# Performance work log

Hardware: AMD Instinct MI355X
Metric: run time of the kernel (lower is better)

Reference implementation:

```python
import jax, jax.numpy as jnp
import numpy as np

EMBED = 512; HEADS = 16; WIN = 8; SHIFT = 4

def _rel_pos_index(Wh, Ww):
    # WindowMSA.double_step_seq + transpose-sum + flip(1)
    seq1 = np.arange(0, (2 * Ww - 1) * Wh, 2 * Ww - 1)
    seq2 = np.arange(0, Ww)
    coords = (seq1[:, None] + seq2[None, :]).reshape(1, -1)
    idx = coords + coords.T            # (Wh*Ww, Wh*Ww)
    return idx[:, ::-1].copy()

def _attn_mask(H_pad, W_pad, win, shift, nf):
    # static (trace-time) shifted-window mask, values in {0, -100}
    img = np.zeros((H_pad, W_pad))
    cnt = 0
    for h in (slice(0, -win), slice(-win, -shift), slice(-shift, None)):
        for w in (slice(0, -win), slice(-win, -shift), slice(-shift, None)):
            img[h, w] = cnt
            cnt += 1
    mw = img.reshape(H_pad // win, win, W_pad // win, win).transpose(0, 2, 1, 3).reshape(-1, win * win)
    am = mw[:, None, :] - mw[:, :, None]
    am = np.where(am != 0, -100.0, 0.0)
    return np.tile(am, (1, 1, nf))     # (nW, N, nf*N)

def setup_inputs():
    key = jax.random.key(0)
    ks = jax.random.split(key, 8)
    B, H, W, C, nf = 8, 128, 128, EMBED, 2
    s = 0.02
    return {
        'q': jax.random.normal(ks[0], (B, H * W, C), jnp.float32),
        'kv': jax.random.normal(ks[1], (B, nf, H * W, C), jnp.float32),
        'H': H, 'W': W,
        'rpb_table': jax.random.normal(ks[2], ((2 * WIN - 1) ** 2, HEADS), jnp.float32) * s,
        'Wq': jax.random.normal(ks[3], (C, C), jnp.float32) * s,
        'bq': jnp.zeros((C,), jnp.float32),
        'Wkv': jax.random.normal(ks[4], (C, 2 * C), jnp.float32) * s,
        'bkv': jnp.zeros((2 * C,), jnp.float32),
        'Wo': jax.random.normal(ks[5], (C, C), jnp.float32) * s,
        'bo': jnp.zeros((C,), jnp.float32),
    }

def reference(q, kv, H, W, rpb_table, Wq, bq, Wkv, bkv, Wo, bo):
    B, L, C = q.shape
    nf = kv.shape[1]
    win, shift, heads = WIN, SHIFT, HEADS
    hd = C // heads
    scale = hd ** -0.5
    pad_b = (-H) % win
    pad_r = (-W) % win
    x = q.reshape(B, H, W, C)
    kvx = kv.reshape(B * nf, H, W, C)
    x = jnp.pad(x, ((0, 0), (0, pad_b), (0, pad_r), (0, 0)))
    kvx = jnp.pad(kvx, ((0, 0), (0, pad_b), (0, pad_r), (0, 0)))
    Hp, Wp = H + pad_b, W + pad_r
    nh, nw = Hp // win, Wp // win
    if shift > 0:
        x = jnp.roll(x, (-shift, -shift), (1, 2))
        kvx = jnp.roll(kvx, (-shift, -shift), (1, 2))
        mask = jnp.asarray(_attn_mask(Hp, Wp, win, shift, nf), q.dtype)
    else:
        mask = None
    Nq = win * win
    Nk = nf * Nq
    # window partition: (B, Hp, Wp, C) -> (B*nh*nw, Nq, C)
    qw = x.reshape(B, nh, win, nw, win, C).transpose(0, 1, 3, 2, 4, 5).reshape(B * nh * nw, Nq, C)
    # kv: (B*nf, Hp, Wp, C) -> (B*nh*nw, nf*Nq, C)
    kvw = kvx.reshape(B, nf, nh, win, nw, win, C).transpose(0, 2, 4, 1, 3, 5, 6).reshape(B * nh * nw, Nk, C)
    Bw = qw.shape[0]
    qh = (qw @ Wq + bq).reshape(Bw, Nq, heads, hd).transpose(0, 2, 1, 3) * scale
    kvp = (kvw @ Wkv + bkv).reshape(Bw, Nk, 2, heads, hd).transpose(2, 0, 3, 1, 4)
    kh, vh = kvp[0], kvp[1]
    attn = jnp.einsum('bhqd,bhkd->bhqk', qh, kh)
    rpi = jnp.asarray(_rel_pos_index(win, win).reshape(-1))
    rpb = rpb_table[rpi].reshape(Nq, Nq, heads).transpose(2, 0, 1)  # (heads, Nq, Nq)
    attn = attn + jnp.tile(rpb, (1, 1, nf))[None]
    if mask is not None:
        nW = mask.shape[0]
        attn = (attn.reshape(Bw // nW, nW, heads, Nq, Nk) + mask[None, :, None]).reshape(Bw, heads, Nq, Nk)
    attn = jax.nn.softmax(attn, axis=-1)
    ow = jnp.einsum('bhqk,bhkd->bqhd', attn, vh).reshape(Bw, Nq, C)
    ow = ow @ Wo + bo
    # window reverse
    x = ow.reshape(B, nh, nw, win, win, C).transpose(0, 1, 3, 2, 4, 5).reshape(B, Hp, Wp, C)
    if shift > 0:
        x = jnp.roll(x, (shift, shift), (1, 2))
    x = x[:, :H, :W, :].reshape(B, H * W, C)
    return x
```

## Files before the change

kernel.cpp:

```cpp
#include <hip/hip_runtime.h>

typedef unsigned short ushort_t;
typedef short bf16x8 __attribute__((ext_vector_type(8)));
typedef float f32x4 __attribute__((ext_vector_type(4)));

#define MFMA16(a, b, c) __builtin_amdgcn_mfma_f32_16x16x32_bf16(a, b, c, 0, 0, 0)

static __device__ __forceinline__ float bf2f(ushort_t u) {
  union { unsigned int i; float f; } v;
  v.i = ((unsigned int)u) << 16;
  return v.f;
}
static __device__ __forceinline__ ushort_t f2bf(float f) {
  union { float f; unsigned int i; } v;
  v.f = f;
  unsigned int u = v.i;
  u = u + 0x7fffu + ((u >> 16) & 1u);
  return (ushort_t)(u >> 16);
}
static __device__ __forceinline__ unsigned int cvtpk(float lo, float hi) {
  unsigned int r;
  asm("v_cvt_pk_bf16_f32 %0, %1, %2" : "=v"(r) : "v"(lo), "v"(hi));
  return r;
}
static __device__ __forceinline__ void gload16(const void* g, void* l) {
  __builtin_amdgcn_global_load_lds((const __attribute__((address_space(1))) void*)g,
                                   (__attribute__((address_space(3))) void*)l,
                                   16, 0, 0);
}

__global__ void ws_sentinel(float* out, unsigned long long ws) {
  if (blockIdx.x == 0 && threadIdx.x == 0)
    out[0] = 1.0e6f * (1.0f + (float)(ws >> 23));
}

__global__ __launch_bounds__(256) void wtrans3(const float* __restrict__ Wq,
                                               const float* __restrict__ Wkv,
                                               const float* __restrict__ Wo,
                                               ushort_t* __restrict__ WqT,
                                               ushort_t* __restrict__ WkvT,
                                               ushort_t* __restrict__ WoT) {
  int idx = blockIdx.x * 256 + threadIdx.x;
  if (idx < 262144) {
    int r = idx >> 9, c = idx & 511;
    WqT[c * 512 + r] = f2bf(Wq[idx]);
  } else if (idx < 786432) {
    int i = idx - 262144;
    int r = i >> 10, c = i & 1023;
    WkvT[c * 512 + r] = f2bf(Wkv[i]);
  } else if (idx < 1048576) {
    int i = idx - 786432;
    int r = i >> 9, c = i & 511;
    WoT[c * 512 + r] = f2bf(Wo[i]);
  }
}

template <bool AF32, bool CF32>
__global__ __launch_bounds__(256, 2) void gemm_bt(const void* __restrict__ Av,
                                                  const ushort_t* __restrict__ Bt,
                                                  const float* __restrict__ bias,
                                                  void* __restrict__ Cv,
                                                  int N, int Nt, float cscale) {
  constexpr int K = 512;
  constexpr int NT = K / 32;
  __shared__ __align__(16) ushort_t As[2][128 * 32];
  __shared__ __align__(16) ushort_t Bs[2][128 * 32];
  const int t = threadIdx.x;
  const int l = t & 63;
  const int w = t >> 6;
  const int w32 = w * 32;
  const int wr = w >> 1, wc = w & 1;
  const int lrow = l & 15;
  const int g = l >> 4;

  const int bid = blockIdx.x;
  const int xcd = bid & 7;
  const int slot = bid >> 3;
  const int mt = xcd + 8 * (slot / Nt);
  const int nt = slot % Nt;
  const long m0 = (long)mt * 128;
  const int n0 = nt * 128;

  const int srow = l >> 2;
  const int sseg = l & 3;
  const int swz = ((srow & 3) << 3);
  const int bcol = (sseg * 8) ^ swz;
  const int acolw = (sseg * 8) ^ swz;

  auto stageB = [&](int buf, int kk) {
#pragma unroll
    for (int i = 0; i < 2; i++) {
      const ushort_t* gp = Bt + (long)(n0 + w32 + i * 16 + srow) * K + kk + bcol;
      gload16(gp, &Bs[buf][(w32 + i * 16) * 32]);
    }
  };
  auto loadA = [&](int kk, f32x4* xf, bf16x8* xb) {
    if constexpr (AF32) {
#pragma unroll
      for (int i = 0; i < 2; i++) {
        const float* gp = (const float*)Av + (m0 + w32 + i * 16 + srow) * (long)K + kk + sseg * 8;
        xf[2 * i] = *(const f32x4*)gp;
        xf[2 * i + 1] = *(const f32x4*)(gp + 4);
      }
    } else {
#pragma unroll
      for (int i = 0; i < 2; i++) {
        const ushort_t* gp = (const ushort_t*)Av + (m0 + w32 + i * 16 + srow) * (long)K + kk + sseg * 8;
        xb[i] = *(const bf16x8*)gp;
      }
    }
  };
  auto writeA = [&](int buf, const f32x4* xf, const bf16x8* xb) {
    if constexpr (AF32) {
#pragma unroll
      for (int i = 0; i < 2; i++) {
        union { unsigned int u[4]; bf16x8 v; } r;
        r.u[0] = cvtpk(xf[2 * i][0], xf[2 * i][1]);
        r.u[1] = cvtpk(xf[2 * i][2], xf[2 * i][3]);
        r.u[2] = cvtpk(xf[2 * i + 1][0], xf[2 * i + 1][1]);
        r.u[3] = cvtpk(xf[2 * i + 1][2], xf[2 * i + 1][3]);
        *(bf16x8*)&As[buf][(w32 + i * 16 + srow) * 32 + acolw] = r.v;
      }
    } else {
#pragma unroll
      for (int i = 0; i < 2; i++)
        *(bf16x8*)&As[buf][(w32 + i * 16 + srow) * 32 + acolw] = xb[i];
    }
  };

  const f32x4 fz = {0.f, 0.f, 0.f, 0.f};
  f32x4 acc[4][4];
#pragma unroll
  for (int i = 0; i < 4; i++)
#pragma unroll
    for (int j = 0; j < 4; j++) acc[i][j] = fz;

  {
#pragma unroll
    for (int tt = 0; tt < 2; tt++) {
      const int kk = tt * 32;
      if constexpr (AF32) {
        f32x4 xf[4];
        loadA(kk, xf, nullptr);
        writeA(tt, xf, nullptr);
      } else {
        bf16x8 xb[2];
        loadA(kk, nullptr, xb);
        writeA(tt, nullptr, xb);
      }
      stageB(tt, kk);
    }
    __syncthreads();
  }

  f32x4 axf[2][4];
  bf16x8 axb[2][2];
  loadA(2 * 32, axf[0], axb[0]);

#pragma unroll
  for (int ts = 0; ts < NT; ++ts) {
    const int cur = ts & 1;
    const int pw = ts & 1;
    const int pl = (ts + 1) & 1;

    if (ts + 3 < NT) loadA((ts + 3) * 32, axf[pl], axb[pl]);

    bf16x8 af[4], bfr[4];
#pragma unroll
    for (int mi = 0; mi < 4; mi++) {
      const int aR = wr * 64 + mi * 16 + lrow;
      af[mi] = *(const bf16x8*)&As[cur][aR * 32 + ((g * 8) ^ ((aR & 3) << 3))];
    }
#pragma unroll
    for (int ni = 0; ni < 4; ni++) {
      const int bR = wc * 64 + ni * 16 + lrow;
      bfr[ni] = *(const bf16x8*)&Bs[cur][bR * 32 + ((g * 8) ^ ((bR & 3) << 3))];
    }
    __builtin_amdgcn_s_setprio(1);
#pragma unroll
    for (int mi = 0; mi < 4; mi++)
#pragma unroll
      for (int ni = 0; ni < 4; ni++)
        acc[mi][ni] = MFMA16(af[mi], bfr[ni], acc[mi][ni]);
    __builtin_amdgcn_s_setprio(0);

    __builtin_amdgcn_sched_barrier(0);
    __builtin_amdgcn_s_barrier();
    __builtin_amdgcn_sched_barrier(0);

    if (ts + 2 < NT) {
      writeA(cur, axf[pw], axb[pw]);
      stageB(cur, (ts + 2) * 32);
      if (ts + 3 < NT) {
        if constexpr (AF32) asm volatile("s_waitcnt vmcnt(6) lgkmcnt(0)" ::: "memory");
        else                asm volatile("s_waitcnt vmcnt(4) lgkmcnt(0)" ::: "memory");
      } else {
        asm volatile("s_waitcnt vmcnt(2) lgkmcnt(0)" ::: "memory");
      }
    } else {
      asm volatile("s_waitcnt vmcnt(0) lgkmcnt(0)" ::: "memory");
    }
    __builtin_amdgcn_sched_barrier(0);
    __builtin_amdgcn_s_barrier();
    __builtin_amdgcn_sched_barrier(0);
  }

#pragma unroll
  for (int mi = 0; mi < 4; mi++) {
    const long row0 = m0 + wr * 64 + mi * 16 + (l >> 4) * 4;
#pragma unroll
    for (int ni = 0; ni < 4; ni++) {
      const int col = n0 + wc * 64 + ni * 16 + lrow;
      const float bv = bias[col];
      if constexpr (CF32) {
#pragma unroll
        for (int r = 0; r < 4; r++)
          ((float*)Cv)[(row0 + r) * N + col] = (acc[mi][ni][r] + bv) * cscale;
      } else {
#pragma unroll
        for (int r = 0; r < 4; r += 2) {
          const float a0 = (acc[mi][ni][r] + bv) * cscale;
          const float a1 = (acc[mi][ni][r + 1] + bv) * cscale;
          const unsigned int pk = cvtpk(a0, a1);
          ((ushort_t*)Cv)[(row0 + r) * N + col] = (ushort_t)(pk & 0xffffu);
          ((ushort_t*)Cv)[(row0 + r + 1) * N + col] = (ushort_t)(pk >> 16);
        }
      }
    }
  }
}

__global__ __launch_bounds__(256, 1) void attn_k(const ushort_t* __restrict__ Qp,
                                                 const ushort_t* __restrict__ KVp,
                                                 const float* __restrict__ rpbt,
                                                 ushort_t* __restrict__ Ao) {
  __shared__ ushort_t P[64 * 136];
  __shared__ ushort_t Ks[128 * 32];
  __shared__ ushort_t Vt[32 * 136];
  __shared__ float Ltab[225];
  const int t = threadIdx.x;
  const int l = t & 63;
  const int w = t >> 6;
  const int wnd = blockIdx.x;
  const int h = blockIdx.y;
  const int b = wnd >> 8;
  const int wh = (wnd >> 4) & 15;
  const int ww = wnd & 15;

  const int lrow = l & 15;
  const int lq = l >> 4;
  const int lk = lq * 8;

  auto qrow = [&](int q) -> long {
    int i = q >> 3, j = q & 7;
    int ho = (wh * 8 + i + 4) & 127;
    int wo = (ww * 8 + j + 4) & 127;
    return (long)((b << 14) + (ho << 7) + wo);
  };
  auto kvrow = [&](int kp) -> long {
    int f = kp >> 6, m = kp & 63;
    int i = m >> 3, j = m & 7;
    int ho = (wh * 8 + i + 4) & 127;
    int wo = (ww * 8 + j + 4) & 127;
    return (long)(((b * 2 + f) << 14) + (ho << 7) + wo);
  };
  auto cnt_of = [&](int m) -> int {
    int hr = wh * 8 + (m >> 3), wr2 = ww * 8 + (m & 7);
    int rh = hr < 120 ? 0 : (hr < 124 ? 1 : 2);
    int rw = wr2 < 120 ? 0 : (wr2 < 124 ? 1 : 2);
    return rh * 3 + rw;
  };
  auto cvec = [](int m) -> int { return 15 * (m >> 3) + (m & 7); };

#pragma unroll
  for (int i = 0; i < 2; i++) {
    const int row = w * 32 + i * 16 + (l >> 2);
    const ushort_t* gp = KVp + kvrow(row) * 1024 + h * 32 + (l & 3) * 8;
    gload16(gp, Ks + (w * 32 + i * 16) * 32);
  }
  {
    const int vkp = t & 127;
    const int vdh = t >> 7;
    const ushort_t* vsrc = KVp + kvrow(vkp) * 1024 + 512 + h * 32 + vdh * 16;
    bf16x8 v0 = *(const bf16x8*)(vsrc);
    bf16x8 v1 = *(const bf16x8*)(vsrc + 8);
#pragma unroll
    for (int d = 0; d < 8; d++) {
      Vt[(vdh * 16 + d) * 136 + vkp] = (ushort_t)v0[d];
      Vt[(vdh * 16 + 8 + d) * 136 + vkp] = (ushort_t)v1[d];
    }
  }
  for (int i = t; i < 225; i += 256) Ltab[i] = rpbt[i * 16 + h];

  bf16x8 af = *(const bf16x8*)(Qp + qrow(w * 16 + lrow) * 512 + h * 32 + lk);

  int ck[8], lidx[8];
#pragma unroll
  for (int ni = 0; ni < 8; ni++) {
    const int k63 = (ni * 16 + lrow) & 63;
    ck[ni] = cnt_of(k63);
    lidx[ni] = cvec(63 - k63);
  }
  int cq4[4], cqv4[4];
#pragma unroll
  for (int r = 0; r < 4; r++) {
    const int q = w * 16 + lq * 4 + r;
    cq4[r] = cnt_of(q);
    cqv4[r] = cvec(q);
  }

  __syncthreads();

  const f32x4 fz = {0.f, 0.f, 0.f, 0.f};
  f32x4 s[8];
#pragma unroll
  for (int ni = 0; ni < 8; ni++) s[ni] = fz;
#pragma unroll
  for (int ni = 0; ni < 8; ni++) {
    bf16x8 kf = *(const bf16x8*)&Ks[(ni * 16 + lrow) * 32 + lk];
    s[ni] = MFMA16(af, kf, s[ni]);
  }

  float inv4[4];
#pragma unroll
  for (int r = 0; r < 4; r++) {
    float mx = -3.0e38f;
#pragma unroll
    for (int ni = 0; ni < 8; ni++) {
      float v = s[ni][r] + Ltab[cqv4[r] + lidx[ni]];
      if (ck[ni] != cq4[r]) v -= 100.f;
      s[ni][r] = v;
      mx = fmaxf(mx, v);
    }
    mx = fmaxf(mx, __shfl_xor(mx, 1));
    mx = fmaxf(mx, __shfl_xor(mx, 2));
    mx = fmaxf(mx, __shfl_xor(mx, 4));
    mx = fmaxf(mx, __shfl_xor(mx, 8));
    float sum = 0.f;
#pragma unroll
    for (int ni = 0; ni < 8; ni++) {
      float p = __expf(s[ni][r] - mx);
      s[ni][r] = p;
      sum += p;
    }
    sum += __shfl_xor(sum, 1);
    sum += __shfl_xor(sum, 2);
    sum += __shfl_xor(sum, 4);
    sum += __shfl_xor(sum, 8);
    inv4[r] = 1.f / sum;
    const int q = w * 16 + lq * 4 + r;
#pragma unroll
    for (int ni = 0; ni < 8; ni += 2) {
      const unsigned int pk = cvtpk(s[ni][r], s[ni + 1][r]);
      P[q * 136 + ni * 16 + lrow] = (ushort_t)(pk & 0xffffu);
      P[q * 136 + (ni + 1) * 16 + lrow] = (ushort_t)(pk >> 16);
    }
  }


  f32x4 o[2] = {fz, fz};
#pragma unroll
  for (int ks = 0; ks < 4; ks++) {
    bf16x8 pf = *(const bf16x8*)&P[(w * 16 + lrow) * 136 + ks * 32 + lk];
#pragma unroll
    for (int ni = 0; ni < 2; ni++) {
      bf16x8 vf = *(const bf16x8*)&Vt[(ni * 16 + lrow) * 136 + ks * 32 + lk];
      o[ni] = MFMA16(pf, vf, o[ni]);
    }
  }

#pragma unroll
  for (int ni = 0; ni < 2; ni++)
#pragma unroll
    for (int r = 0; r < 4; r += 2) {
      const unsigned int pk = cvtpk(o[ni][r] * inv4[r], o[ni][r + 1] * inv4[r + 1]);
      const int q0 = w * 16 + lq * 4 + r;
      Ao[qrow(q0) * 512 + h * 32 + ni * 16 + lrow] = (ushort_t)(pk & 0xffffu);
      Ao[qrow(q0 + 1) * 512 + h * 32 + ni * 16 + lrow] = (ushort_t)(pk >> 16);
    }
}

extern "C" void kernel_launch(void* const* d_in, const int* in_sizes, int n_in,
                              void* d_out, int out_size, void* d_ws, size_t ws_size,
                              hipStream_t stream) {
  (void)in_sizes; (void)n_in; (void)out_size;
  const float* q    = (const float*)d_in[0];
  const float* kv   = (const float*)d_in[1];
  const float* rpbt = (const float*)d_in[4];
  const float* Wq   = (const float*)d_in[5];
  const float* bq   = (const float*)d_in[6];
  const float* Wkv  = (const float*)d_in[7];
  const float* bkv  = (const float*)d_in[8];
  const float* Wo   = (const float*)d_in[9];
  const float* bo   = (const float*)d_in[10];
  float* out = (float*)d_out;

  const size_t QB  = 16384ULL * 512;
  const size_t KVB = 32768ULL * 1024;
  const size_t per_b_bytes = (QB + QB + KVB) * 2;
  const size_t fixed_bytes = (512ULL*512 + 512ULL*1024 + 512ULL*512) * 2;
  const size_t needed1 = fixed_bytes + per_b_bytes;

  if (ws_size < needed1) {
    ws_sentinel<<<dim3(1), 64, 0, stream>>>(out, (unsigned long long)ws_size);
    return;
  }

  int nbc = 8;
  while (nbc > 1 && fixed_bytes + (size_t)nbc * per_b_bytes > ws_size) nbc >>= 1;

  char* ws = (char*)d_ws;
  ushort_t* WqT  = (ushort_t*)ws;
  ushort_t* WkvT = WqT + 512 * 512;
  ushort_t* WoT  = WkvT + 512 * 1024;
  ushort_t* Qp   = (ushort_t*)(ws + fixed_bytes);
  ushort_t* Ao   = Qp + (size_t)nbc * QB;
  ushort_t* KVp  = Ao + (size_t)nbc * QB;

  wtrans3<<<dim3(4096), 256, 0, stream>>>(Wq, Wkv, Wo, WqT, WkvT, WoT);

  const float scale = 0.17677669529663687f;
  for (int c = 0; c < 8 / nbc; ++c) {
    const size_t b0 = (size_t)c * nbc;
    const int MtQ = nbc * 128;
    const int MtKV = nbc * 256;
    gemm_bt<true, false><<<dim3(MtQ * 4), 256, 0, stream>>>(q + b0 * QB, WqT, bq,
                                                            Qp, 512, 4, scale);
    gemm_bt<true, false><<<dim3(MtKV * 8), 256, 0, stream>>>(kv + b0 * KVB / 2, WkvT,
                                                             bkv, KVp, 1024, 8, 1.0f);
    attn_k<<<dim3(nbc * 256, 16), 256, 0, stream>>>(Qp, KVp, rpbt, Ao);
    gemm_bt<false, true><<<dim3(MtQ * 4), 256, 0, stream>>>(Ao, WoT, bo,
                                                            out + b0 * QB, 512, 4, 1.0f);
  }
}
```

Baseline: 1.030 ms.

## Restructure GEMM main loop to single-barrier double-buffered pipeline

Reworks the K-loop software pipeline of the projection GEMM. Each iteration now writes the next LDS buffer and issues the next global prefetch before computing on the current buffer, using one barrier per iteration instead of two. The register staging drops from two prefetch slots to one, and the loop is no longer force-unrolled. This aims to cut barrier stalls and register pressure, at the cost of a shallower global-load prefetch distance and possible LDS write/read conflicts if the wait counts are wrong.

New measurement: 1.057 ms. +2.6%, slower.

```diff
diff --git a/kernel.cpp b/kernel.cpp
--- a/kernel.cpp
+++ b/kernel.cpp
@@ -135,35 +135,27 @@
 #pragma unroll
     for (int j = 0; j < 4; j++) acc[i][j] = fz;
 
-  {
-#pragma unroll
-    for (int tt = 0; tt < 2; tt++) {
-      const int kk = tt * 32;
-      if constexpr (AF32) {
-        f32x4 xf[4];
-        loadA(kk, xf, nullptr);
-        writeA(tt, xf, nullptr);
-      } else {
-        bf16x8 xb[2];
-        loadA(kk, nullptr, xb);
-        writeA(tt, nullptr, xb);
-      }
-      stageB(tt, kk);
-    }
-    __syncthreads();
-  }
-
-  f32x4 axf[2][4];
-  bf16x8 axb[2][2];
-  loadA(2 * 32, axf[0], axb[0]);
-
-#pragma unroll
+  f32x4 axf[4];
+  bf16x8 axb[2];
+
+  loadA(0, axf, axb);
+  writeA(0, axf, axb);
+  stageB(0, 0);
+  loadA(32, axf, axb);
+  if constexpr (AF32) asm volatile("s_waitcnt vmcnt(4) lgkmcnt(0)" ::: "memory");
+  else                asm volatile("s_waitcnt vmcnt(2) lgkmcnt(0)" ::: "memory");
+  __builtin_amdgcn_sched_barrier(0);
+  __builtin_amdgcn_s_barrier();
+  __builtin_amdgcn_sched_barrier(0);
+
   for (int ts = 0; ts < NT; ++ts) {
     const int cur = ts & 1;
-    const int pw = ts & 1;
-    const int pl = (ts + 1) & 1;
-
-    if (ts + 3 < NT) loadA((ts + 3) * 32, axf[pl], axb[pl]);
+
+    if (ts + 1 < NT) {
+      writeA(cur ^ 1, axf, axb);
+      stageB(cur ^ 1, (ts + 1) * 32);
+    }
+    if (ts + 2 < NT) loadA((ts + 2) * 32, axf, axb);
 
     bf16x8 af[4], bfr[4];
 #pragma unroll
@@ -184,25 +176,17 @@
         acc[mi][ni] = MFMA16(af[mi], bfr[ni], acc[mi][ni]);
     __builtin_amdgcn_s_setprio(0);
 
-    __builtin_amdgcn_sched_barrier(0);
-    __builtin_amdgcn_s_barrier();
-    __builtin_amdgcn_sched_barrier(0);
-
-    if (ts + 2 < NT) {
-      writeA(cur, axf[pw], axb[pw]);
-      stageB(cur, (ts + 2) * 32);
-      if (ts + 3 < NT) {
-        if constexpr (AF32) asm volatile("s_waitcnt vmcnt(6) lgkmcnt(0)" ::: "memory");
-        else                asm volatile("s_waitcnt vmcnt(4) lgkmcnt(0)" ::: "memory");
+    if (ts + 1 < NT) {
+      if (ts + 2 < NT) {
+        if constexpr (AF32) asm volatile("s_waitcnt vmcnt(4) lgkmcnt(0)" ::: "memory");
+        else                asm volatile("s_waitcnt vmcnt(2) lgkmcnt(0)" ::: "memory");
       } else {
-        asm volatile("s_waitcnt vmcnt(2) lgkmcnt(0)" ::: "memory");
+        asm volatile("s_waitcnt vmcnt(0) lgkmcnt(0)" ::: "memory");
       }
-    } else {
-      asm volatile("s_waitcnt vmcnt(0) lgkmcnt(0)" ::: "memory");
-    }
-    __builtin_amdgcn_sched_barrier(0);
-    __builtin_amdgcn_s_barrier();
-    __builtin_amdgcn_sched_barrier(0);
+      __builtin_amdgcn_sched_barrier(0);
+      __builtin_amdgcn_s_barrier();
+      __builtin_amdgcn_sched_barrier(0);
+    }
   }
 
 #pragma unroll
```
